# Optimization experiments

Measured on AMD Instinct MI355X. Metric: run time of the kernel, lower is better.

The kernel has to match this reference:

```python
import jax, jax.numpy as jnp
import numpy as np

B, V, CODE_NUM = 64, 100, 4096
CODE_SIZE, ATT, VISIT, TIME, HID, OUT = 256, 128, 256, 64, 512, 90
TYPE_NUM = 32
NEG = -2.0 ** 31


def setup_inputs() -> dict:
    key = jax.random.key(0)
    ks = jax.random.split(key, 24)
    s = 0.02
    return {
        'code_x': jax.random.randint(ks[0], (B, V, CODE_NUM), 0, 2).astype(jnp.float32),
        'code_type0': jax.random.randint(ks[1], (CODE_NUM + 1,), 0, TYPE_NUM),
        'code_type1': jax.random.randint(ks[2], (CODE_NUM + 1,), 0, TYPE_NUM),
        'code_type2': jax.random.randint(ks[3], (CODE_NUM + 1,), 0, TYPE_NUM),
        'lens': jax.random.randint(ks[4], (B,), 1, V + 1),
        'intervals': jax.random.uniform(ks[5], (B, V), dtype=jnp.float32),
        # encoder: code + 3 type embedding tables (rows 1..code_num used)
        'code_emb': jax.random.normal(ks[6], (CODE_NUM + 1, CODE_SIZE), jnp.float32) * s,
        't0_emb': jax.random.normal(ks[7], (TYPE_NUM, CODE_SIZE), jnp.float32) * s,
        't1_emb': jax.random.normal(ks[8], (TYPE_NUM, CODE_SIZE), jnp.float32) * s,
        't2_emb': jax.random.normal(ks[9], (TYPE_NUM, CODE_SIZE), jnp.float32) * s,
        # visit self-attention (no bias, per nn.Linear(..., bias=False))
        'Wq': jax.random.normal(ks[10], (CODE_SIZE, ATT), jnp.float32) * s,
        'Wk': jax.random.normal(ks[11], (CODE_SIZE, ATT), jnp.float32) * s,
        'Wv': jax.random.normal(ks[12], (CODE_SIZE, VISIT), jnp.float32) * s,
        # time embedding Linear(1, time_size)
        'time_w': jax.random.normal(ks[13], (TIME,), jnp.float32) * s,
        'time_b': jnp.zeros((TIME,), jnp.float32),
        # GRUCell params (torch layout: gates ordered r,z,n)
        'gru_Wih': jax.random.normal(ks[14], (3 * HID, VISIT + TIME), jnp.float32) * s,
        'gru_Whh': jax.random.normal(ks[15], (3 * HID, HID), jnp.float32) * s,
        'gru_bih': jnp.zeros((3 * HID,), jnp.float32),
        'gru_bhh': jnp.zeros((3 * HID,), jnp.float32),
        # classifier
        'cls_W': jax.random.normal(ks[16], (OUT, HID), jnp.float32) * s,
        'cls_b': jnp.zeros((OUT,), jnp.float32),
    }


def reference(code_x, code_type0, code_type1, code_type2, lens, intervals,
              code_emb, t0_emb, t1_emb, t2_emb, Wq, Wk, Wv, time_w, time_b,
              gru_Wih, gru_Whh, gru_bih, gru_bhh, cls_W, cls_b):
    # --- Encoder (vectorized): multi-hot slot i corresponds to code id i+1 ---
    E = (code_emb[1:]
         + t0_emb[code_type0[1:]]
         + t1_emb[code_type1[1:]]
         + t2_emb[code_type2[1:]])                      # [CODE_NUM, CODE_SIZE]
    active = (code_x > 0).astype(E.dtype)               # [B, V, CODE_NUM]
    counts = jnp.maximum(active.sum(-1, keepdims=True), 1.0)
    v_emb_ini = jnp.einsum('bvc,cd->bvd', active, E) / counts  # mean over codes
    visit_mask = jnp.arange(V)[None, :] < lens[:, None]        # [B, V]
    v_emb_ini = v_emb_ini * visit_mask[..., None]              # padded visits stay 0

    # --- Context-aware visit self-attention ---
    Q = v_emb_ini @ Wq                                   # [B, V, ATT]
    K = v_emb_ini @ Wk
    Vv = v_emb_ini @ Wv                                  # [B, V, VISIT]
    alpha = jnp.einsum('bqa,bka->bqk', Q, K)
    alpha = jnp.where(visit_mask[:, None, :], alpha, NEG)  # mask keys
    alpha = jax.nn.softmax(alpha, axis=2)
    v_emb = jnp.einsum('bqk,bkd->bqd', alpha, Vv) + Vv     # [B, V, VISIT]

    # --- Time-aware input ---
    t_emb = intervals[..., None] * time_w + time_b         # [B, V, TIME]
    x = jnp.concatenate([v_emb, t_emb], axis=-1)           # [B, V, VISIT+TIME]

    # --- GRU over visits, gated by per-patient length ---
    def step(h, xm):
        xt, mt = xm                                        # xt [B,D], mt [B]
        gi = xt @ gru_Wih.T + gru_bih
        gh = h @ gru_Whh.T + gru_bhh
        ir, iz, inn = jnp.split(gi, 3, axis=-1)
        hr, hz, hn = jnp.split(gh, 3, axis=-1)
        r = jax.nn.sigmoid(ir + hr)
        z = jax.nn.sigmoid(iz + hz)
        n = jnp.tanh(inn + r * hn)
        h_new = (1.0 - z) * n + z * h
        h = jnp.where(mt[:, None], h_new, h)
        return h, None

    h0 = jnp.zeros((B, HID), x.dtype)
    h_final, _ = jax.lax.scan(step, h0, (x.transpose(1, 0, 2), visit_mask.T))

    # --- Classifier (dropout p=0 -> identity) ---
    return jax.nn.sigmoid(h_final @ cls_W.T + cls_b)       # [B, OUT]
```

## Files before the change

### kernel.cpp

```cpp
#include <hip/hip_runtime.h>
#include <hip/hip_bf16.h>

typedef float  f32x4 __attribute__((ext_vector_type(4)));
typedef short  s16x8 __attribute__((ext_vector_type(8)));

#define NEGBIG -1e30f

__device__ __forceinline__ unsigned short f2b(float f) {
    union { float f; unsigned u; } c; c.f = f;
    unsigned r = c.u + 0x7FFF + ((c.u >> 16) & 1);
    return (unsigned short)(r >> 16);
}
__device__ __forceinline__ float b2f(unsigned short h) {
    union { unsigned u; float f; } c; c.u = ((unsigned)h) << 16;
    return c.f;
}
__device__ __forceinline__ float sigm(float x) { return 1.f / (1.f + __expf(-x)); }

__device__ __forceinline__ s16x8 ld_b128_sc(const unsigned short* p) {
    s16x8 r;
    asm volatile("global_load_dwordx4 %0, %1, off sc0 sc1" : "=v"(r) : "v"(p));
    return r;
}
__device__ __forceinline__ void st_short_sc(unsigned short* p, unsigned short v) {
    unsigned int dv = v;
    asm volatile("global_store_short %0, %1, off sc0 sc1" :: "v"(p), "v"(dv) : "memory");
}

#define POLL_H(BASE, AF) do {                                                        \
    unsigned okm_ = 0; int guard_ = 0;                                               \
    while (true) {                                                                   \
        _Pragma("unroll")                                                            \
        for (int kk_ = 0; kk_ < 16; ++kk_)                                           \
            if (!((okm_ >> kk_) & 1)) AF[kk_] = ld_b128_sc((BASE) + kk_ * 32);       \
        asm volatile("s_waitcnt vmcnt(0)" ::: "memory");                             \
        __builtin_amdgcn_sched_barrier(0);                                           \
        _Pragma("unroll")                                                            \
        for (int kk_ = 0; kk_ < 16; ++kk_) if (!((okm_ >> kk_) & 1)) {               \
            bool bad_ = false;                                                       \
            _Pragma("unroll")                                                        \
            for (int e_ = 0; e_ < 8; ++e_)                                           \
                bad_ = bad_ || ((unsigned short)AF[kk_][e_] == (unsigned short)0xFFFFu); \
            if (!bad_) okm_ |= (1u << kk_);                                          \
        }                                                                            \
        if (__all(okm_ == 0xFFFFu)) break;                                           \
        if (++guard_ > (1 << 18)) break;                        \
    }                                                                                \
    __builtin_amdgcn_sched_barrier(0);                                               \
} while (0)

__global__ void init_zero(int* flags, unsigned short* hb0, unsigned short* hb1, unsigned short* hb2) {
    int idx = blockIdx.x * 256 + threadIdx.x;
    int stride = gridDim.x * 256;
    for (int i = idx; i < 1024; i += stride) flags[i] = 0;
    for (int i = idx; i < 32768; i += stride) {
        hb0[i] = 0;
        hb1[i] = 0xFFFFu;
        hb2[i] = 0xFFFFu;
    }
}

__global__ void prep_w(const float* Wq, const float* Wk, const float* Wv,
                       const float* gWih, const float* gWhh,
                       unsigned short* wcat, unsigned short* wih, unsigned short* whh) {
    int idx = blockIdx.x * 256 + threadIdx.x;
    int stride = gridDim.x * 256;
    const int N1 = 131072, N2 = 491520, N3 = 786432;
    for (; idx < N1 + N2 + N3; idx += stride) {
        if (idx < N1) {
            int n = idx >> 8, k = idx & 255;
            float v;
            if (n < 128) v = Wq[k * 128 + n];
            else if (n < 256) v = Wk[k * 128 + (n - 128)];
            else v = Wv[k * 256 + (n - 256)];
            wcat[n * 256 + k] = f2b(v);
        } else if (idx < N1 + N2) {
            int i = idx - N1; wih[i] = f2b(gWih[i]);
        } else {
            int i = idx - N1 - N2; whh[i] = f2b(gWhh[i]);
        }
    }
}

__global__ __launch_bounds__(256) void prep_et(const float* code_emb, const int* ct0, const int* ct1, const int* ct2,
                                               const float* t0e, const float* t1e, const float* t2e,
                                               unsigned short* ET) {
    __shared__ float tile[64][65];
    const int d0 = blockIdx.x * 64, c0 = blockIdx.y * 64;
    const int t = threadIdx.x;
    for (int p = 0; p < 16; ++p) {
        int idx = p * 256 + t;
        int dl = idx & 63, cl = idx >> 6;
        int code = c0 + cl + 1;
        int d = d0 + dl;
        float v = code_emb[code * 256 + d] + t0e[ct0[code] * 256 + d]
                + t1e[ct1[code] * 256 + d] + t2e[ct2[code] * 256 + d];
        tile[dl][cl] = v;
    }
    __syncthreads();
    for (int p = 0; p < 2; ++p) {
        int idx = p * 256 + t;
        int dl = idx >> 3, ch = idx & 7;
        s16x8 pk;
#pragma unroll
        for (int e = 0; e < 8; ++e) pk[e] = (short)f2b(tile[dl][ch * 8 + e]);
        *(s16x8*)(ET + (size_t)(d0 + dl) * 4096 + c0 + ch * 8) = pk;
    }
}

__global__ __launch_bounds__(256) void enc_gemm(const float* code_x, const unsigned short* ET,
                                                const int* lens, unsigned short* Vb) {
    __shared__ __align__(16) char sm[4096 + 32768 + 128];
    char* As = sm;
    char* Bs = sm + 4096;
    float* cl = (float*)(sm + 4096 + 32768);
    const int m0 = blockIdx.x * 32;
    const int t = threadIdx.x, l = t & 63, w = t >> 6;
    const int lr = l & 15, lq = l >> 4, l7 = l & 7;
    const int sr = t >> 3, sc = t & 7;
    f32x4 acc[2][4];
#pragma unroll
    for (int a = 0; a < 2; ++a)
#pragma unroll
        for (int b = 0; b < 4; ++b) acc[a][b] = (f32x4){0.f, 0.f, 0.f, 0.f};
    int cnt = 0;
    for (int it = 0; it < 64; ++it) {
        const int k0 = it * 64;
        const float* ga = code_x + (size_t)(m0 + sr) * 4096 + k0 + sc * 8;
        f32x4 a0 = *(const f32x4*)ga;
        f32x4 a1 = *(const f32x4*)(ga + 4);
        s16x8 ap;
#pragma unroll
        for (int e = 0; e < 4; ++e) { bool on = a0[e] > 0.f; ap[e] = on ? (short)0x3F80 : (short)0; cnt += on ? 1 : 0; }
#pragma unroll
        for (int e = 0; e < 4; ++e) { bool on = a1[e] > 0.f; ap[4 + e] = on ? (short)0x3F80 : (short)0; cnt += on ? 1 : 0; }
        *(s16x8*)(As + sr * 128 + ((sc ^ (sr & 7)) << 4)) = ap;
#pragma unroll
        for (int rd = 0; rd < 8; ++rd) {
            int i = rd * 256 + t;
            int n = i >> 3, cc = i & 7;
            s16x8 bv = *(const s16x8*)(ET + (size_t)n * 4096 + k0 + cc * 8);
            *(s16x8*)(Bs + n * 128 + ((cc ^ (n & 7)) << 4)) = bv;
        }
        __syncthreads();
#pragma unroll
        for (int kk = 0; kk < 2; ++kk) {
            const int cp = kk * 4 + lq;
            s16x8 af[2], bf[4];
#pragma unroll
            for (int mt = 0; mt < 2; ++mt)
                af[mt] = *(const s16x8*)(As + (mt * 16 + lr) * 128 + ((cp ^ l7) << 4));
#pragma unroll
            for (int nt = 0; nt < 4; ++nt)
                bf[nt] = *(const s16x8*)(Bs + ((w * 4 + nt) * 16 + lr) * 128 + ((cp ^ l7) << 4));
#pragma unroll
            for (int mt = 0; mt < 2; ++mt)
#pragma unroll
                for (int nt = 0; nt < 4; ++nt)
                    acc[mt][nt] = __builtin_amdgcn_mfma_f32_16x16x32_bf16(af[mt], bf[nt], acc[mt][nt], 0, 0, 0);
        }
        __syncthreads();
    }
    float fc = (float)cnt;
    fc += __shfl_xor(fc, 1); fc += __shfl_xor(fc, 2); fc += __shfl_xor(fc, 4);
    if (sc == 0) cl[sr] = fmaxf(fc, 1.f);
    __syncthreads();
#pragma unroll
    for (int mt = 0; mt < 2; ++mt)
#pragma unroll
        for (int i = 0; i < 4; ++i) {
            int m = mt * 16 + lq * 4 + i;
            int gm = m0 + m;
            float rc = 1.f / cl[m];
            unsigned bi = (unsigned)gm / 100u;
            unsigned vi = (unsigned)gm - bi * 100u;
            float msk = ((int)vi < lens[bi]) ? 1.f : 0.f;
#pragma unroll
            for (int nt = 0; nt < 4; ++nt) {
                int n = (w * 4 + nt) * 16 + lr;
                Vb[(size_t)gm * 256 + n] = f2b(acc[mt][nt][i] * rc * msk);
            }
        }
}

__global__ __launch_bounds__(256) void gemm_bf16(const unsigned short* A, const unsigned short* Bm,
                                                 int K, int Ntot, int mode,
                                                 unsigned short* outp, const float* bias) {
    __shared__ __align__(16) char sm[4096 + 32768];
    char* As = sm;
    char* Bs = sm + 4096;
    const int m0 = blockIdx.x * 32;
    const int n0 = blockIdx.y * 256;
    const int t = threadIdx.x, l = t & 63, w = t >> 6;
    const int lr = l & 15, lq = l >> 4, l7 = l & 7;
    const int sr = t >> 3, sc = t & 7;
    const int iters = K >> 6;
    f32x4 acc[2][4];
#pragma unroll
    for (int a = 0; a < 2; ++a)
#pragma unroll
        for (int b = 0; b < 4; ++b) acc[a][b] = (f32x4){0.f, 0.f, 0.f, 0.f};
    for (int it = 0; it < iters; ++it) {
        const int k0 = it * 64;
        s16x8 av = *(const s16x8*)(A + (size_t)(m0 + sr) * K + k0 + sc * 8);
        *(s16x8*)(As + sr * 128 + ((sc ^ (sr & 7)) << 4)) = av;
#pragma unroll
        for (int rd = 0; rd < 8; ++rd) {
            int i = rd * 256 + t;
            int n = i >> 3, cc = i & 7;
            s16x8 bv = *(const s16x8*)(Bm + (size_t)(n0 + n) * K + k0 + cc * 8);
            *(s16x8*)(Bs + n * 128 + ((cc ^ (n & 7)) << 4)) = bv;
        }
        __syncthreads();
#pragma unroll
        for (int kk = 0; kk < 2; ++kk) {
            const int cp = kk * 4 + lq;
            s16x8 af[2], bf[4];
#pragma unroll
            for (int mt = 0; mt < 2; ++mt)
                af[mt] = *(const s16x8*)(As + (mt * 16 + lr) * 128 + ((cp ^ l7) << 4));
#pragma unroll
            for (int nt = 0; nt < 4; ++nt)
                bf[nt] = *(const s16x8*)(Bs + ((w * 4 + nt) * 16 + lr) * 128 + ((cp ^ l7) << 4));
#pragma unroll
            for (int mt = 0; mt < 2; ++mt)
#pragma unroll
                for (int nt = 0; nt < 4; ++nt)
                    acc[mt][nt] = __builtin_amdgcn_mfma_f32_16x16x32_bf16(af[mt], bf[nt], acc[mt][nt], 0, 0, 0);
        }
        __syncthreads();
    }
#pragma unroll
    for (int mt = 0; mt < 2; ++mt)
#pragma unroll
        for (int i = 0; i < 4; ++i) {
            int gm = m0 + mt * 16 + lq * 4 + i;
#pragma unroll
            for (int nt = 0; nt < 4; ++nt) {
                int n = n0 + (w * 4 + nt) * 16 + lr;
                float v = acc[mt][nt][i];
                if (mode == 1) v += bias[n];
                outp[(size_t)gm * Ntot + n] = f2b(v);
            }
        }
}

__global__ __launch_bounds__(256) void attn_kernel(const unsigned short* QKV, const int* lens,
                                                   const float* intervals, const float* time_w, const float* time_b,
                                                   unsigned short* X) {
    __shared__ __align__(16) char sm[28672 + 32768];
    char* Pb = sm;
    char* VTb = sm + 28672;
    const int b = blockIdx.x;
    const int t = threadIdx.x, l = t & 63, w = t >> 6;
    const int lr = l & 15, lq = l >> 4;
    const int lenb = lens[b];
    for (int p = 0; p < 7; ++p) {
        int idx = p * 256 + t;
        *(f32x4*)(Pb + idx * 16) = (f32x4){0.f, 0.f, 0.f, 0.f};
    }
    __syncthreads();
    f32x4 S[2][7];
#pragma unroll
    for (int a = 0; a < 2; ++a)
#pragma unroll
        for (int c = 0; c < 7; ++c) S[a][c] = (f32x4){0.f, 0.f, 0.f, 0.f};
#pragma unroll
    for (int kk = 0; kk < 4; ++kk) {
        s16x8 qa[2], kb[7];
#pragma unroll
        for (int mi = 0; mi < 2; ++mi) {
            int mt = 2 * w + mi;
            if (mt > 6) continue;
            int row = b * 100 + mt * 16 + lr;
            qa[mi] = *(const s16x8*)(QKV + (size_t)row * 512 + kk * 32 + lq * 8);
        }
#pragma unroll
        for (int nt = 0; nt < 7; ++nt) {
            int row = b * 100 + nt * 16 + lr;
            kb[nt] = *(const s16x8*)(QKV + (size_t)row * 512 + 128 + kk * 32 + lq * 8);
        }
#pragma unroll
        for (int mi = 0; mi < 2; ++mi) {
            int mt = 2 * w + mi;
            if (mt > 6) continue;
#pragma unroll
            for (int nt = 0; nt < 7; ++nt)
                S[mi][nt] = __builtin_amdgcn_mfma_f32_16x16x32_bf16(qa[mi], kb[nt], S[mi][nt], 0, 0, 0);
        }
    }
#pragma unroll
    for (int mi = 0; mi < 2; ++mi) {
        int mt = 2 * w + mi;
        if (mt > 6) continue;
        float sv[7][4];
#pragma unroll
        for (int nt = 0; nt < 7; ++nt) {
            int j = nt * 16 + lr;
#pragma unroll
            for (int i = 0; i < 4; ++i)
                sv[nt][i] = (j < lenb) ? S[mi][nt][i] : NEGBIG;
        }
#pragma unroll
        for (int i = 0; i < 4; ++i) {
            float mx = sv[0][i];
#pragma unroll
            for (int nt = 1; nt < 7; ++nt) mx = fmaxf(mx, sv[nt][i]);
            mx = fmaxf(mx, __shfl_xor(mx, 1));
            mx = fmaxf(mx, __shfl_xor(mx, 2));
            mx = fmaxf(mx, __shfl_xor(mx, 4));
            mx = fmaxf(mx, __shfl_xor(mx, 8));
            float e[7], sum = 0.f;
#pragma unroll
            for (int nt = 0; nt < 7; ++nt) { e[nt] = __expf(sv[nt][i] - mx); sum += e[nt]; }
            sum += __shfl_xor(sum, 1);
            sum += __shfl_xor(sum, 2);
            sum += __shfl_xor(sum, 4);
            sum += __shfl_xor(sum, 8);
            float rs = 1.f / sum;
            int m = mt * 16 + lq * 4 + i;
#pragma unroll
            for (int nt = 0; nt < 7; ++nt) {
                int j = nt * 16 + lr;
                *(unsigned short*)(Pb + m * 256 + (((j >> 3) ^ (m & 7)) << 4) + ((j & 7) << 1)) = f2b(e[nt] * rs);
            }
        }
    }
    __syncthreads();
    for (int h = 0; h < 2; ++h) {
        for (int p = 0; p < 8; ++p) {
            int idx = p * 256 + t;
            *(f32x4*)(VTb + idx * 16) = (f32x4){0.f, 0.f, 0.f, 0.f};
        }
        __syncthreads();
        for (int p = 0; p < 7; ++p) {
            int ci = p * 256 + t;
            if (ci < 1600) {
                int j = ci >> 4, d8 = ci & 15;
                s16x8 vv = *(const s16x8*)(QKV + (size_t)(b * 100 + j) * 512 + 256 + h * 128 + d8 * 8);
#pragma unroll
                for (int e = 0; e < 8; ++e) {
                    int dl = d8 * 8 + e;
                    *(unsigned short*)(VTb + dl * 256 + (((j >> 3) ^ (dl & 7)) << 4) + ((j & 7) << 1)) = (unsigned short)vv[e];
                }
            }
        }
        __syncthreads();
        f32x4 O[2][8];
#pragma unroll
        for (int a = 0; a < 2; ++a)
#pragma unroll
            for (int c = 0; c < 8; ++c) O[a][c] = (f32x4){0.f, 0.f, 0.f, 0.f};
#pragma unroll
        for (int kk = 0; kk < 4; ++kk) {
            s16x8 pa[2];
#pragma unroll
            for (int mi = 0; mi < 2; ++mi) {
                int mt = 2 * w + mi;
                if (mt > 6) continue;
                int m = mt * 16 + lr;
                pa[mi] = *(const s16x8*)(Pb + m * 256 + (((kk * 4 + lq) ^ (m & 7)) << 4));
            }
#pragma unroll
            for (int nt = 0; nt < 8; ++nt) {
                int dl = nt * 16 + lr;
                s16x8 vb = *(const s16x8*)(VTb + dl * 256 + (((kk * 4 + lq) ^ (dl & 7)) << 4));
#pragma unroll
                for (int mi = 0; mi < 2; ++mi) {
                    int mt = 2 * w + mi;
                    if (mt > 6) continue;
                    O[mi][nt] = __builtin_amdgcn_mfma_f32_16x16x32_bf16(pa[mi], vb, O[mi][nt], 0, 0, 0);
                }
            }
        }
#pragma unroll
        for (int mi = 0; mi < 2; ++mi) {
            int mt = 2 * w + mi;
            if (mt > 6) continue;
#pragma unroll
            for (int i = 0; i < 4; ++i) {
                int m = mt * 16 + lq * 4 + i;
                if (m < 100) {
#pragma unroll
                    for (int nt = 0; nt < 8; ++nt) {
                        int dl = nt * 16 + lr;
                        float res = b2f(*(unsigned short*)(VTb + dl * 256 + (((m >> 3) ^ (dl & 7)) << 4) + ((m & 7) << 1)));
                        X[(size_t)(b * 100 + m) * 320 + h * 128 + dl] = f2b(O[mi][nt][i] + res);
                    }
                }
            }
        }
        if (h == 0) __syncthreads();
    }
    for (int p = 0; p < 25; ++p) {
        int idx = p * 256 + t;
        int m = idx >> 6, d = idx & 63;
        float val = intervals[b * 100 + m] * time_w[d] + time_b[d];
        X[(size_t)(b * 100 + m) * 320 + 256 + d] = f2b(val);
    }
}

__global__ __launch_bounds__(256, 1) void gru_kernel(const unsigned short* GIb, const unsigned short* WHH,
                                                     const float* gbhh, const int* lens,
                                                     unsigned short* hbA, unsigned short* hbB, unsigned short* hbC,
                                                     const float* clsW, const float* clsb, float* out) {
    const int bid = blockIdx.x;
    const int t = threadIdx.x, l = t & 63, w = t >> 6;
    const int lr = l & 15, lq = l >> 4;
    const int j = bid * 16 + lr;
    int ml;
    {
        int v = lens[l];
        v = max(v, __shfl_xor(v, 1));  v = max(v, __shfl_xor(v, 2));
        v = max(v, __shfl_xor(v, 4));  v = max(v, __shfl_xor(v, 8));
        v = max(v, __shfl_xor(v, 16)); v = max(v, __shfl_xor(v, 32));
        ml = v;
    }
    int lens4[4];
#pragma unroll
    for (int i = 0; i < 4; ++i) lens4[i] = lens[w * 16 + lq * 4 + i];
    const float bhr = gbhh[j], bhz = gbhh[512 + j], bhn = gbhh[1024 + j];
    s16x8 Bf[3][16];
#pragma unroll
    for (int g = 0; g < 3; ++g)
#pragma unroll
        for (int kk = 0; kk < 16; ++kk)
            Bf[g][kk] = *(const s16x8*)(WHH + (size_t)(g * 512 + j) * 512 + kk * 32 + lq * 8);
    float ho[4] = {0.f, 0.f, 0.f, 0.f};
    size_t gi_base[4];
    size_t hrow[4];
#pragma unroll
    for (int i = 0; i < 4; ++i) {
        gi_base[i] = (size_t)((w * 16 + lq * 4 + i) * 100) * 1536 + j;
        hrow[i]    = (size_t)(w * 16 + lq * 4 + i) * 512 + j;
    }
    const size_t arow = (size_t)(w * 16 + lr) * 512 + lq * 8;

    float gir[4], giz[4], gin[4];
#pragma unroll
    for (int i = 0; i < 4; ++i) {
        const unsigned short* gp = GIb + gi_base[i];
        gir[i] = b2f(gp[0]); giz[i] = b2f(gp[512]); gin[i] = b2f(gp[1024]);
    }

    unsigned short* rb = hbA;
    unsigned short* wb = hbB;
    unsigned short* pb = hbC;

    for (int step = 0; step < ml; ++step) {
        s16x8 af[16];
        POLL_H(rb + arow, af);
#pragma unroll
        for (int i = 0; i < 4; ++i) st_short_sc(pb + hrow[i], (unsigned short)0xFFFFu);
        f32x4 ar = (f32x4){0.f,0.f,0.f,0.f}, az = ar, an = ar;
#pragma unroll
        for (int kk = 0; kk < 16; ++kk) {
            ar = __builtin_amdgcn_mfma_f32_16x16x32_bf16(af[kk], Bf[0][kk], ar, 0, 0, 0);
            az = __builtin_amdgcn_mfma_f32_16x16x32_bf16(af[kk], Bf[1][kk], az, 0, 0, 0);
            an = __builtin_amdgcn_mfma_f32_16x16x32_bf16(af[kk], Bf[2][kk], an, 0, 0, 0);
        }
#pragma unroll
        for (int i = 0; i < 4; ++i) {
            float r = sigm(gir[i] + ar[i] + bhr);
            float z = sigm(giz[i] + az[i] + bhz);
            float n = tanhf(gin[i] + r * (an[i] + bhn));
            float hv = (step < lens4[i]) ? ((1.f - z) * n + z * ho[i]) : ho[i];
            ho[i] = hv;
            st_short_sc(wb + hrow[i], f2b(hv));
        }
        if (step + 1 < ml) {
#pragma unroll
            for (int i = 0; i < 4; ++i) {
                const unsigned short* gp = GIb + gi_base[i] + (size_t)(step + 1) * 1536;
                gir[i] = b2f(gp[0]); giz[i] = b2f(gp[512]); gin[i] = b2f(gp[1024]);
            }
        }
        unsigned short* tmp = rb; rb = wb; wb = pb; pb = tmp;
    }

    if (bid < 30) {
        {
            s16x8 af[16];
            POLL_H(rb + arow, af);
        }
        const unsigned short* fbuf = rb;
        int bb = t >> 2, qq = t & 3;
        int c0 = bid * 3;
        float s0 = 0.f, s1 = 0.f, s2 = 0.f;
        for (int kc = 0; kc < 16; ++kc) {
            int k = qq * 128 + kc * 8;
            s16x8 hvb = *(const s16x8*)(fbuf + (size_t)bb * 512 + k);
            f32x4 w0a = *(const f32x4*)(clsW + (size_t)(c0 + 0) * 512 + k);
            f32x4 w0b = *(const f32x4*)(clsW + (size_t)(c0 + 0) * 512 + k + 4);
            f32x4 w1a = *(const f32x4*)(clsW + (size_t)(c0 + 1) * 512 + k);
            f32x4 w1b = *(const f32x4*)(clsW + (size_t)(c0 + 1) * 512 + k + 4);
            f32x4 w2a = *(const f32x4*)(clsW + (size_t)(c0 + 2) * 512 + k);
            f32x4 w2b = *(const f32x4*)(clsW + (size_t)(c0 + 2) * 512 + k + 4);
#pragma unroll
            for (int e = 0; e < 4; ++e) {
                float h0 = b2f((unsigned short)hvb[e]);
                float h1 = b2f((unsigned short)hvb[4 + e]);
                s0 += h0 * w0a[e] + h1 * w0b[e];
                s1 += h0 * w1a[e] + h1 * w1b[e];
                s2 += h0 * w2a[e] + h1 * w2b[e];
            }
        }
        s0 += __shfl_xor(s0, 1); s0 += __shfl_xor(s0, 2);
        s1 += __shfl_xor(s1, 1); s1 += __shfl_xor(s1, 2);
        s2 += __shfl_xor(s2, 1); s2 += __shfl_xor(s2, 2);
        if (qq == 0) {
            out[bb * 90 + c0 + 0] = sigm(s0 + clsb[c0 + 0]);
            out[bb * 90 + c0 + 1] = sigm(s1 + clsb[c0 + 1]);
            out[bb * 90 + c0 + 2] = sigm(s2 + clsb[c0 + 2]);
        }
    }
}

extern "C" void kernel_launch(void* const* d_in, const int* in_sizes, int n_in,
                              void* d_out, int out_size, void* d_ws, size_t ws_size,
                              hipStream_t stream) {
    const float* code_x   = (const float*)d_in[0];
    const int*   ct0      = (const int*)d_in[1];
    const int*   ct1      = (const int*)d_in[2];
    const int*   ct2      = (const int*)d_in[3];
    const int*   lens     = (const int*)d_in[4];
    const float* intervals= (const float*)d_in[5];
    const float* code_emb = (const float*)d_in[6];
    const float* t0e      = (const float*)d_in[7];
    const float* t1e      = (const float*)d_in[8];
    const float* t2e      = (const float*)d_in[9];
    const float* Wq       = (const float*)d_in[10];
    const float* Wk       = (const float*)d_in[11];
    const float* Wv       = (const float*)d_in[12];
    const float* time_w   = (const float*)d_in[13];
    const float* time_b   = (const float*)d_in[14];
    const float* gWih     = (const float*)d_in[15];
    const float* gWhh     = (const float*)d_in[16];
    const float* gbih     = (const float*)d_in[17];
    const float* gbhh     = (const float*)d_in[18];
    const float* clsW     = (const float*)d_in[19];
    const float* clsb     = (const float*)d_in[20];

    char* ws = (char*)d_ws;
    const size_t ET_OFF   = 0;
    const size_t WCAT_OFF = 2097152;
    const size_t WIH_OFF  = 2359296;
    const size_t WHH_OFF  = 3342336;
    const size_t V_OFF    = 4915200;
    const size_t QKV_OFF  = 8192000;
    const size_t X_OFF    = 14778368;
    const size_t GI_OFF   = 18874368;
    const size_t HB0_OFF  = 38535168;
    const size_t HB1_OFF  = 38600704;
    const size_t HB2_OFF  = 38666240;
    const size_t FLG_OFF  = 38797312;

    unsigned short* ET   = (unsigned short*)(ws + ET_OFF);
    unsigned short* WCAT = (unsigned short*)(ws + WCAT_OFF);
    unsigned short* WIH  = (unsigned short*)(ws + WIH_OFF);
    unsigned short* WHH  = (unsigned short*)(ws + WHH_OFF);
    unsigned short* Vb   = (unsigned short*)(ws + V_OFF);
    unsigned short* QKV  = (unsigned short*)(ws + QKV_OFF);
    unsigned short* Xb   = (unsigned short*)(ws + X_OFF);
    unsigned short* GIb  = (unsigned short*)(ws + GI_OFF);
    unsigned short* hb0  = (unsigned short*)(ws + HB0_OFF);
    unsigned short* hb1  = (unsigned short*)(ws + HB1_OFF);
    unsigned short* hb2  = (unsigned short*)(ws + HB2_OFF);
    int*            flags= (int*)(ws + FLG_OFF);

    init_zero<<<8, 256, 0, stream>>>(flags, hb0, hb1, hb2);
    prep_w<<<512, 256, 0, stream>>>(Wq, Wk, Wv, gWih, gWhh, WCAT, WIH, WHH);
    prep_et<<<dim3(4, 64), 256, 0, stream>>>(code_emb, ct0, ct1, ct2, t0e, t1e, t2e, ET);
    enc_gemm<<<200, 256, 0, stream>>>(code_x, ET, lens, Vb);
    gemm_bf16<<<dim3(200, 2), 256, 0, stream>>>(Vb, WCAT, 256, 512, 2, QKV, nullptr);
    attn_kernel<<<64, 256, 0, stream>>>(QKV, lens, intervals, time_w, time_b, Xb);
    gemm_bf16<<<dim3(200, 6), 256, 0, stream>>>(Xb, WIH, 320, 1536, 1, GIb, gbih);
    gru_kernel<<<32, 256, 0, stream>>>(GIb, WHH, gbhh, lens, hb0, hb1, hb2, clsW, clsb, (float*)d_out);
}
```

Measured before the change: 858.4 us.

## Replace sentinel-polling triple buffer with per-wave step flags and double buffer

The GRU recurrence previously spun on the hidden-state data itself, using a 0xFFFF sentinel across three rotating buffers, and re-invalidated one buffer every step. It now uses two ping-pong buffers. Each wave publishes a per-wave step counter after its stores drain, and waits with s_sleep backoff until all 128 wave flags reach the current step before reading h. This removes the repeated wide sentinel reloads and the invalidation stores, at the cost of a full all-wave barrier each step and the latency of a flag round trip. It relies on relaxed atomics plus vmcnt waits and sc0/sc1 loads for ordering.

New measurement: 768.9 us. 10.4% less time.

```diff
diff --git a/kernel.cpp b/kernel.cpp
--- a/kernel.cpp
+++ b/kernel.cpp
@@ -27,37 +27,11 @@
     asm volatile("global_store_short %0, %1, off sc0 sc1" :: "v"(p), "v"(dv) : "memory");
 }
 
-#define POLL_H(BASE, AF) do {                                                        \
-    unsigned okm_ = 0; int guard_ = 0;                                               \
-    while (true) {                                                                   \
-        _Pragma("unroll")                                                            \
-        for (int kk_ = 0; kk_ < 16; ++kk_)                                           \
-            if (!((okm_ >> kk_) & 1)) AF[kk_] = ld_b128_sc((BASE) + kk_ * 32);       \
-        asm volatile("s_waitcnt vmcnt(0)" ::: "memory");                             \
-        __builtin_amdgcn_sched_barrier(0);                                           \
-        _Pragma("unroll")                                                            \
-        for (int kk_ = 0; kk_ < 16; ++kk_) if (!((okm_ >> kk_) & 1)) {               \
-            bool bad_ = false;                                                       \
-            _Pragma("unroll")                                                        \
-            for (int e_ = 0; e_ < 8; ++e_)                                           \
-                bad_ = bad_ || ((unsigned short)AF[kk_][e_] == (unsigned short)0xFFFFu); \
-            if (!bad_) okm_ |= (1u << kk_);                                          \
-        }                                                                            \
-        if (__all(okm_ == 0xFFFFu)) break;                                           \
-        if (++guard_ > (1 << 18)) break;                        \
-    }                                                                                \
-    __builtin_amdgcn_sched_barrier(0);                                               \
-} while (0)
-
-__global__ void init_zero(int* flags, unsigned short* hb0, unsigned short* hb1, unsigned short* hb2) {
+__global__ void init_zero(int* flags, unsigned short* hb0) {
     int idx = blockIdx.x * 256 + threadIdx.x;
     int stride = gridDim.x * 256;
     for (int i = idx; i < 1024; i += stride) flags[i] = 0;
-    for (int i = idx; i < 32768; i += stride) {
-        hb0[i] = 0;
-        hb1[i] = 0xFFFFu;
-        hb2[i] = 0xFFFFu;
-    }
+    for (int i = idx; i < 32768; i += stride) hb0[i] = 0;
 }
 
 __global__ void prep_w(const float* Wq, const float* Wk, const float* Wv,
@@ -402,8 +376,8 @@
 
 __global__ __launch_bounds__(256, 1) void gru_kernel(const unsigned short* GIb, const unsigned short* WHH,
                                                      const float* gbhh, const int* lens,
-                                                     unsigned short* hbA, unsigned short* hbB, unsigned short* hbC,
-                                                     const float* clsW, const float* clsb, float* out) {
+                                                     unsigned short* hb0, unsigned short* hb1,
+                                                     int* flags, const float* clsW, const float* clsb, float* out) {
     const int bid = blockIdx.x;
     const int t = threadIdx.x, l = t & 63, w = t >> 6;
     const int lr = l & 15, lq = l >> 4;
@@ -435,6 +409,7 @@
         hrow[i]    = (size_t)(w * 16 + lq * 4 + i) * 512 + j;
     }
     const size_t arow = (size_t)(w * 16 + lr) * 512 + lq * 8;
+    const int myflag = (bid * 4 + w) * 8;
 
     float gir[4], giz[4], gin[4];
 #pragma unroll
@@ -443,15 +418,20 @@
         gir[i] = b2f(gp[0]); giz[i] = b2f(gp[512]); gin[i] = b2f(gp[1024]);
     }
 
-    unsigned short* rb = hbA;
-    unsigned short* wb = hbB;
-    unsigned short* pb = hbC;
-
     for (int step = 0; step < ml; ++step) {
+        const unsigned short* hb = (step & 1) ? hb1 : hb0;
+        unsigned short* hn = (step & 1) ? hb0 : hb1;
+#pragma unroll
+        for (int g = 0; g < 3; ++g)
+#pragma unroll
+            for (int kk = 0; kk < 16; ++kk)
+                asm volatile("" : "+v"(Bf[g][kk]));
         s16x8 af[16];
-        POLL_H(rb + arow, af);
-#pragma unroll
-        for (int i = 0; i < 4; ++i) st_short_sc(pb + hrow[i], (unsigned short)0xFFFFu);
+#pragma unroll
+        for (int kk = 0; kk < 16; ++kk)
+            af[kk] = ld_b128_sc(hb + arow + kk * 32);
+        asm volatile("s_waitcnt vmcnt(0)" ::: "memory");
+        __builtin_amdgcn_sched_barrier(0);
         f32x4 ar = (f32x4){0.f,0.f,0.f,0.f}, az = ar, an = ar;
 #pragma unroll
         for (int kk = 0; kk < 16; ++kk) {
@@ -466,8 +446,11 @@
             float n = tanhf(gin[i] + r * (an[i] + bhn));
             float hv = (step < lens4[i]) ? ((1.f - z) * n + z * ho[i]) : ho[i];
             ho[i] = hv;
-            st_short_sc(wb + hrow[i], f2b(hv));
-        }
+            st_short_sc(hn + hrow[i], f2b(hv));
+        }
+        asm volatile("s_waitcnt vmcnt(0)" ::: "memory");
+        if (l == 0)
+            __hip_atomic_store(flags + myflag, step + 1, __ATOMIC_RELAXED, __HIP_MEMORY_SCOPE_AGENT);
         if (step + 1 < ml) {
 #pragma unroll
             for (int i = 0; i < 4; ++i) {
@@ -475,15 +458,37 @@
                 gir[i] = b2f(gp[0]); giz[i] = b2f(gp[512]); gin[i] = b2f(gp[1024]);
             }
         }
-        unsigned short* tmp = rb; rb = wb; wb = pb; pb = tmp;
+        {
+            int guard = 0;
+            while (true) {
+                int v = (l < 32) ? __hip_atomic_load(flags + (l * 4 + w) * 8, __ATOMIC_RELAXED, __HIP_MEMORY_SCOPE_AGENT) : (step + 1);
+                if (__all(v >= step + 1)) break;
+                if (++guard > (1 << 20)) break;
+                __builtin_amdgcn_s_sleep(1);
+            }
+        }
+        __builtin_amdgcn_sched_barrier(0);
     }
 
     if (bid < 30) {
         {
-            s16x8 af[16];
-            POLL_H(rb + arow, af);
-        }
-        const unsigned short* fbuf = rb;
+            int guard = 0;
+            while (true) {
+                int v = ml;
+                if (l < 32) {
+                    int v0 = __hip_atomic_load(flags + (l * 4 + 0) * 8, __ATOMIC_RELAXED, __HIP_MEMORY_SCOPE_AGENT);
+                    int v1 = __hip_atomic_load(flags + (l * 4 + 1) * 8, __ATOMIC_RELAXED, __HIP_MEMORY_SCOPE_AGENT);
+                    int v2 = __hip_atomic_load(flags + (l * 4 + 2) * 8, __ATOMIC_RELAXED, __HIP_MEMORY_SCOPE_AGENT);
+                    int v3 = __hip_atomic_load(flags + (l * 4 + 3) * 8, __ATOMIC_RELAXED, __HIP_MEMORY_SCOPE_AGENT);
+                    v = min(min(v0, v1), min(v2, v3));
+                }
+                if (__all(v >= ml)) break;
+                if (++guard > (1 << 20)) break;
+                __builtin_amdgcn_s_sleep(1);
+            }
+        }
+        __builtin_amdgcn_sched_barrier(0);
+        const unsigned short* fbuf = (ml & 1) ? hb1 : hb0;
         int bb = t >> 2, qq = t & 3;
         int c0 = bid * 3;
         float s0 = 0.f, s1 = 0.f, s2 = 0.f;
@@ -552,7 +557,6 @@
     const size_t GI_OFF   = 18874368;
     const size_t HB0_OFF  = 38535168;
     const size_t HB1_OFF  = 38600704;
-    const size_t HB2_OFF  = 38666240;
     const size_t FLG_OFF  = 38797312;
 
     unsigned short* ET   = (unsigned short*)(ws + ET_OFF);
@@ -565,15 +569,14 @@
     unsigned short* GIb  = (unsigned short*)(ws + GI_OFF);
     unsigned short* hb0  = (unsigned short*)(ws + HB0_OFF);
     unsigned short* hb1  = (unsigned short*)(ws + HB1_OFF);
-    unsigned short* hb2  = (unsigned short*)(ws + HB2_OFF);
     int*            flags= (int*)(ws + FLG_OFF);
 
-    init_zero<<<8, 256, 0, stream>>>(flags, hb0, hb1, hb2);
+    init_zero<<<8, 256, 0, stream>>>(flags, hb0);
     prep_w<<<512, 256, 0, stream>>>(Wq, Wk, Wv, gWih, gWhh, WCAT, WIH, WHH);
     prep_et<<<dim3(4, 64), 256, 0, stream>>>(code_emb, ct0, ct1, ct2, t0e, t1e, t2e, ET);
     enc_gemm<<<200, 256, 0, stream>>>(code_x, ET, lens, Vb);
     gemm_bf16<<<dim3(200, 2), 256, 0, stream>>>(Vb, WCAT, 256, 512, 2, QKV, nullptr);
     attn_kernel<<<64, 256, 0, stream>>>(QKV, lens, intervals, time_w, time_b, Xb);
     gemm_bf16<<<dim3(200, 6), 256, 0, stream>>>(Xb, WIH, 320, 1536, 1, GIb, gbih);
-    gru_kernel<<<32, 256, 0, stream>>>(GIb, WHH, gbhh, lens, hb0, hb1, hb2, clsW, clsb, (float*)d_out);
-}
+    gru_kernel<<<32, 256, 0, stream>>>(GIb, WHH, gbhh, lens, hb0, hb1, flags, clsW, clsb, (float*)d_out);
+}
```

## Restructure GRU recurrence: LDS weights, transposed MFMA, packed stores, four-buffer ring

Applied to the files above, without the earlier changes.

The GRU kernel now keeps its Whh slice in swizzled shared memory instead of registers and swaps the MFMA operands so each lane owns four consecutive hidden units of one batch row. That allows 64-bit packed stores of the new hidden state and of the invalidation sentinel, plus vectorized loads of the input gates. The ring of hidden-state buffers grows from three to four, which gives more slack before a buffer is reused. Polling now checks two elements per vector and sleeps between retries. The aim is to cut cross-block sync latency and store count per step, at the cost of LDS reads inside the recurrence and a weaker sentinel check.

Result: slower. 875.8 us (+2.0%).

```diff
diff --git a/kernel.cpp b/kernel.cpp
--- a/kernel.cpp
+++ b/kernel.cpp
@@ -3,6 +3,7 @@
 
 typedef float  f32x4 __attribute__((ext_vector_type(4)));
 typedef short  s16x8 __attribute__((ext_vector_type(8)));
+typedef short  s16x4 __attribute__((ext_vector_type(4)));
 
 #define NEGBIG -1e30f
 
@@ -22,9 +23,9 @@
     asm volatile("global_load_dwordx4 %0, %1, off sc0 sc1" : "=v"(r) : "v"(p));
     return r;
 }
-__device__ __forceinline__ void st_short_sc(unsigned short* p, unsigned short v) {
-    unsigned int dv = v;
-    asm volatile("global_store_short %0, %1, off sc0 sc1" :: "v"(p), "v"(dv) : "memory");
+__device__ __forceinline__ void st_b64_sc(unsigned short* p, unsigned int x, unsigned int y) {
+    union { unsigned int u[2]; unsigned long long ull; } v; v.u[0] = x; v.u[1] = y;
+    asm volatile("global_store_dwordx2 %0, %1, off sc0 sc1" :: "v"(p), "v"(v.ull) : "memory");
 }
 
 #define POLL_H(BASE, AF) do {                                                        \
@@ -37,26 +38,25 @@
         __builtin_amdgcn_sched_barrier(0);                                           \
         _Pragma("unroll")                                                            \
         for (int kk_ = 0; kk_ < 16; ++kk_) if (!((okm_ >> kk_) & 1)) {               \
-            bool bad_ = false;                                                       \
-            _Pragma("unroll")                                                        \
-            for (int e_ = 0; e_ < 8; ++e_)                                           \
-                bad_ = bad_ || ((unsigned short)AF[kk_][e_] == (unsigned short)0xFFFFu); \
-            if (!bad_) okm_ |= (1u << kk_);                                          \
+            bool ok_ = ((unsigned short)AF[kk_][0] != (unsigned short)0xFFFFu)       \
+                    && ((unsigned short)AF[kk_][4] != (unsigned short)0xFFFFu);      \
+            if (ok_) okm_ |= (1u << kk_);                                            \
         }                                                                            \
         if (__all(okm_ == 0xFFFFu)) break;                                           \
         if (++guard_ > (1 << 18)) break;                        \
+        __builtin_amdgcn_s_sleep(1);                                                 \
     }                                                                                \
     __builtin_amdgcn_sched_barrier(0);                                               \
 } while (0)
 
-__global__ void init_zero(int* flags, unsigned short* hb0, unsigned short* hb1, unsigned short* hb2) {
+__global__ void init_zero(unsigned short* hb0, unsigned short* hb1, unsigned short* hb2, unsigned short* hb3) {
     int idx = blockIdx.x * 256 + threadIdx.x;
     int stride = gridDim.x * 256;
-    for (int i = idx; i < 1024; i += stride) flags[i] = 0;
     for (int i = idx; i < 32768; i += stride) {
         hb0[i] = 0;
         hb1[i] = 0xFFFFu;
         hb2[i] = 0xFFFFu;
+        hb3[i] = 0xFFFFu;
     }
 }
 
@@ -402,12 +402,22 @@
 
 __global__ __launch_bounds__(256, 1) void gru_kernel(const unsigned short* GIb, const unsigned short* WHH,
                                                      const float* gbhh, const int* lens,
-                                                     unsigned short* hbA, unsigned short* hbB, unsigned short* hbC,
+                                                     unsigned short* hbA, unsigned short* hbB,
+                                                     unsigned short* hbC, unsigned short* hbD,
                                                      const float* clsW, const float* clsb, float* out) {
+    __shared__ __align__(16) char Wlds[49152];
     const int bid = blockIdx.x;
     const int t = threadIdx.x, l = t & 63, w = t >> 6;
-    const int lr = l & 15, lq = l >> 4;
-    const int j = bid * 16 + lr;
+    const int lo = l & 15, hi = l >> 4, lo7 = l & 7;
+    const int batch = w * 16 + lo;
+    const int j0 = bid * 16 + hi * 4;
+    for (int p = 0; p < 12; ++p) {
+        int idx = p * 256 + t;
+        int row = idx >> 6, slot = idx & 63;
+        int g = row >> 4, jl = row & 15;
+        s16x8 v = *(const s16x8*)(WHH + (size_t)(g * 512 + bid * 16 + jl) * 512 + slot * 8);
+        *(s16x8*)(Wlds + row * 1024 + ((slot ^ (jl & 7)) << 4)) = v;
+    }
     int ml;
     {
         int v = lens[l];
@@ -416,74 +426,75 @@
         v = max(v, __shfl_xor(v, 16)); v = max(v, __shfl_xor(v, 32));
         ml = v;
     }
-    int lens4[4];
-#pragma unroll
-    for (int i = 0; i < 4; ++i) lens4[i] = lens[w * 16 + lq * 4 + i];
-    const float bhr = gbhh[j], bhz = gbhh[512 + j], bhn = gbhh[1024 + j];
-    s16x8 Bf[3][16];
-#pragma unroll
-    for (int g = 0; g < 3; ++g)
-#pragma unroll
-        for (int kk = 0; kk < 16; ++kk)
-            Bf[g][kk] = *(const s16x8*)(WHH + (size_t)(g * 512 + j) * 512 + kk * 32 + lq * 8);
+    const int len = lens[batch];
+    const f32x4 bhr4 = *(const f32x4*)(gbhh + j0);
+    const f32x4 bhz4 = *(const f32x4*)(gbhh + 512 + j0);
+    const f32x4 bhn4 = *(const f32x4*)(gbhh + 1024 + j0);
+    __syncthreads();
+
+    const int wb0 = (0 * 16 + lo) * 1024;
+    const int wb1 = (1 * 16 + lo) * 1024;
+    const int wb2 = (2 * 16 + lo) * 1024;
+
     float ho[4] = {0.f, 0.f, 0.f, 0.f};
-    size_t gi_base[4];
-    size_t hrow[4];
-#pragma unroll
-    for (int i = 0; i < 4; ++i) {
-        gi_base[i] = (size_t)((w * 16 + lq * 4 + i) * 100) * 1536 + j;
-        hrow[i]    = (size_t)(w * 16 + lq * 4 + i) * 512 + j;
-    }
-    const size_t arow = (size_t)(w * 16 + lr) * 512 + lq * 8;
-
-    float gir[4], giz[4], gin[4];
-#pragma unroll
-    for (int i = 0; i < 4; ++i) {
-        const unsigned short* gp = GIb + gi_base[i];
-        gir[i] = b2f(gp[0]); giz[i] = b2f(gp[512]); gin[i] = b2f(gp[1024]);
-    }
-
-    unsigned short* rb = hbA;
-    unsigned short* wb = hbB;
-    unsigned short* pb = hbC;
+    const size_t prow = (size_t)batch * 512 + j0;
+    const size_t arow = (size_t)batch * 512 + hi * 8;
+    const size_t gi_row = (size_t)batch * 100;
+
+    s16x4 pgr = *(const s16x4*)(GIb + gi_row * 1536 + j0);
+    s16x4 pgz = *(const s16x4*)(GIb + gi_row * 1536 + 512 + j0);
+    s16x4 pgn = *(const s16x4*)(GIb + gi_row * 1536 + 1024 + j0);
+
+    unsigned short* R = hbA;
+    unsigned short* W = hbB;
+    unsigned short* X = hbC;
+    unsigned short* P = hbD;
 
     for (int step = 0; step < ml; ++step) {
         s16x8 af[16];
-        POLL_H(rb + arow, af);
-#pragma unroll
-        for (int i = 0; i < 4; ++i) st_short_sc(pb + hrow[i], (unsigned short)0xFFFFu);
+        POLL_H(R + arow, af);
+        st_b64_sc(P + prow, 0xFFFFFFFFu, 0xFFFFFFFFu);
         f32x4 ar = (f32x4){0.f,0.f,0.f,0.f}, az = ar, an = ar;
 #pragma unroll
         for (int kk = 0; kk < 16; ++kk) {
-            ar = __builtin_amdgcn_mfma_f32_16x16x32_bf16(af[kk], Bf[0][kk], ar, 0, 0, 0);
-            az = __builtin_amdgcn_mfma_f32_16x16x32_bf16(af[kk], Bf[1][kk], az, 0, 0, 0);
-            an = __builtin_amdgcn_mfma_f32_16x16x32_bf16(af[kk], Bf[2][kk], an, 0, 0, 0);
-        }
-#pragma unroll
-        for (int i = 0; i < 4; ++i) {
-            float r = sigm(gir[i] + ar[i] + bhr);
-            float z = sigm(giz[i] + az[i] + bhz);
-            float n = tanhf(gin[i] + r * (an[i] + bhn));
-            float hv = (step < lens4[i]) ? ((1.f - z) * n + z * ho[i]) : ho[i];
-            ho[i] = hv;
-            st_short_sc(wb + hrow[i], f2b(hv));
-        }
+            const int so = ((kk * 4 + hi) ^ lo7) << 4;
+            s16x8 wr = *(const s16x8*)(Wlds + wb0 + so);
+            s16x8 wz = *(const s16x8*)(Wlds + wb1 + so);
+            s16x8 wn = *(const s16x8*)(Wlds + wb2 + so);
+            ar = __builtin_amdgcn_mfma_f32_16x16x32_bf16(wr, af[kk], ar, 0, 0, 0);
+            az = __builtin_amdgcn_mfma_f32_16x16x32_bf16(wz, af[kk], az, 0, 0, 0);
+            an = __builtin_amdgcn_mfma_f32_16x16x32_bf16(wn, af[kk], an, 0, 0, 0);
+        }
+        unsigned px, py;
+        {
+            float h01[2], h23[2];
+#pragma unroll
+            for (int i = 0; i < 4; ++i) {
+                float r = sigm(b2f((unsigned short)pgr[i]) + ar[i] + bhr4[i]);
+                float z = sigm(b2f((unsigned short)pgz[i]) + az[i] + bhz4[i]);
+                float n = tanhf(b2f((unsigned short)pgn[i]) + r * (an[i] + bhn4[i]));
+                float hv = (step < len) ? ((1.f - z) * n + z * ho[i]) : ho[i];
+                ho[i] = hv;
+                if (i < 2) h01[i] = hv; else h23[i - 2] = hv;
+            }
+            px = (unsigned)f2b(h01[0]) | ((unsigned)f2b(h01[1]) << 16);
+            py = (unsigned)f2b(h23[0]) | ((unsigned)f2b(h23[1]) << 16);
+        }
+        st_b64_sc(W + prow, px, py);
         if (step + 1 < ml) {
-#pragma unroll
-            for (int i = 0; i < 4; ++i) {
-                const unsigned short* gp = GIb + gi_base[i] + (size_t)(step + 1) * 1536;
-                gir[i] = b2f(gp[0]); giz[i] = b2f(gp[512]); gin[i] = b2f(gp[1024]);
-            }
-        }
-        unsigned short* tmp = rb; rb = wb; wb = pb; pb = tmp;
+            pgr = *(const s16x4*)(GIb + (gi_row + step + 1) * 1536 + j0);
+            pgz = *(const s16x4*)(GIb + (gi_row + step + 1) * 1536 + 512 + j0);
+            pgn = *(const s16x4*)(GIb + (gi_row + step + 1) * 1536 + 1024 + j0);
+        }
+        unsigned short* tmp = R; R = W; W = X; X = P; P = tmp;
     }
 
     if (bid < 30) {
         {
             s16x8 af[16];
-            POLL_H(rb + arow, af);
-        }
-        const unsigned short* fbuf = rb;
+            POLL_H(R + arow, af);
+        }
+        const unsigned short* fbuf = R;
         int bb = t >> 2, qq = t & 3;
         int c0 = bid * 3;
         float s0 = 0.f, s1 = 0.f, s2 = 0.f;
@@ -553,7 +564,7 @@
     const size_t HB0_OFF  = 38535168;
     const size_t HB1_OFF  = 38600704;
     const size_t HB2_OFF  = 38666240;
-    const size_t FLG_OFF  = 38797312;
+    const size_t HB3_OFF  = 38731776;
 
     unsigned short* ET   = (unsigned short*)(ws + ET_OFF);
     unsigned short* WCAT = (unsigned short*)(ws + WCAT_OFF);
@@ -566,14 +577,14 @@
     unsigned short* hb0  = (unsigned short*)(ws + HB0_OFF);
     unsigned short* hb1  = (unsigned short*)(ws + HB1_OFF);
     unsigned short* hb2  = (unsigned short*)(ws + HB2_OFF);
-    int*            flags= (int*)(ws + FLG_OFF);
-
-    init_zero<<<8, 256, 0, stream>>>(flags, hb0, hb1, hb2);
+    unsigned short* hb3  = (unsigned short*)(ws + HB3_OFF);
+
+    init_zero<<<8, 256, 0, stream>>>(hb0, hb1, hb2, hb3);
     prep_w<<<512, 256, 0, stream>>>(Wq, Wk, Wv, gWih, gWhh, WCAT, WIH, WHH);
     prep_et<<<dim3(4, 64), 256, 0, stream>>>(code_emb, ct0, ct1, ct2, t0e, t1e, t2e, ET);
     enc_gemm<<<200, 256, 0, stream>>>(code_x, ET, lens, Vb);
     gemm_bf16<<<dim3(200, 2), 256, 0, stream>>>(Vb, WCAT, 256, 512, 2, QKV, nullptr);
     attn_kernel<<<64, 256, 0, stream>>>(QKV, lens, intervals, time_w, time_b, Xb);
     gemm_bf16<<<dim3(200, 6), 256, 0, stream>>>(Xb, WIH, 320, 1536, 1, GIb, gbih);
-    gru_kernel<<<32, 256, 0, stream>>>(GIb, WHH, gbhh, lens, hb0, hb1, hb2, clsW, clsb, (float*)d_out);
-}
+    gru_kernel<<<32, 256, 0, stream>>>(GIb, WHH, gbhh, lens, hb0, hb1, hb2, hb3, clsW, clsb, (float*)d_out);
+}
```
